# Kernel tuning notes

Hardware: AMD Instinct MI355X
Metric: run time of the kernel (lower is better)

## Reference

```python
import jax, jax.numpy as jnp
import numpy as np


def setup_inputs() -> dict:
    key = jax.random.key(0)
    k1, k2, k3 = jax.random.split(key, 3)
    N, F, C, E = 100000, 256, 64, 3200000
    x = jax.random.normal(k1, (N, F), dtype=jnp.float32)
    edge_index = jax.random.randint(k2, (2, E), 0, N, dtype=jnp.int64)
    W = jax.random.normal(k3, (F, C), dtype=jnp.float32) * (1.0 / np.sqrt(F))
    b = jnp.zeros((C,), dtype=jnp.float32)
    return {"x": x, "edge_index": edge_index, "W": W, "b": b}


def reference(x, edge_index, W, b):
    N = x.shape[0]
    # Linear transform first (GCNConv: x @ W)
    xw = x @ W  # [N, C]
    # gcn_norm: add self-loops with weight 1
    loops = jnp.arange(N, dtype=edge_index.dtype)
    src = jnp.concatenate([edge_index[0], loops])
    dst = jnp.concatenate([edge_index[1], loops])
    ones = jnp.ones(src.shape[0], dtype=xw.dtype)
    deg = jax.ops.segment_sum(ones, dst, num_segments=N)  # in-degree incl. self-loop
    deg_inv_sqrt = jnp.where(deg > 0, jax.lax.rsqrt(deg), 0.0)
    norm = deg_inv_sqrt[src] * deg_inv_sqrt[dst]  # [E+N]
    # Message: norm * x_j, then MEAN aggregation over destinations (aggr='mean')
    msg = xw[src] * norm[:, None]  # [E+N, C]
    agg = jax.ops.segment_sum(msg, dst, num_segments=N)  # [N, C]
    cnt = jnp.maximum(deg, 1.0)  # number of incoming messages per node
    out = agg / cnt[:, None] + b
    return jax.nn.log_softmax(out, axis=1)
```

## Files before the change

kernel.cpp:

```cpp
#include <hip/hip_runtime.h>


#define C_DIM 64
#define F_DIM 256
#define TILE 128
#define BIN_PT 16
#define BIN_TILE_E 4096
#define SORT_CAP 6144
#define SMEM_BYTES 36880

typedef __attribute__((ext_vector_type(8))) short bf16x8;
typedef __attribute__((ext_vector_type(2))) short bf16x2;
typedef __attribute__((ext_vector_type(4))) float f32x4;

static __device__ __forceinline__ unsigned short f2bf(float f) {
    unsigned int u = __float_as_uint(f);
    unsigned int r = (u + 0x7FFFu + ((u >> 16) & 1u)) >> 16;
    return (unsigned short)r;
}
static __device__ __forceinline__ float u2lo(unsigned int u) {
    return __uint_as_float(u << 16);
}
static __device__ __forceinline__ float u2hi(unsigned int u) {
    return __uint_as_float(u & 0xFFFF0000u);
}

#if __has_builtin(__builtin_amdgcn_fdot2_f32_bf16)
static __device__ __forceinline__ void acc_pair(unsigned int u, float& lo, float& hi) {
    union { unsigned int ui; bf16x2 v; } p;
    p.ui = u;
    const bf16x2 SEL_LO = { (short)0x3F80, (short)0 };
    const bf16x2 SEL_HI = { (short)0, (short)0x3F80 };
    lo = __builtin_amdgcn_fdot2_f32_bf16(p.v, SEL_LO, lo, false);
    hi = __builtin_amdgcn_fdot2_f32_bf16(p.v, SEL_HI, hi, false);
}
#else
static __device__ __forceinline__ void acc_pair(unsigned int u, float& lo, float& hi) {
    lo += u2lo(u);
    hi += u2hi(u);
}
#endif


__global__ void k_zero1(int* __restrict__ a, int N) {
    int i = blockIdx.x * blockDim.x + threadIdx.x;
    if (i < N) a[i] = 0;
}

__global__ void k_zero2(int* __restrict__ a, int* __restrict__ b, int N) {
    int i = blockIdx.x * blockDim.x + threadIdx.x;
    if (i < N) { a[i] = 0; b[i] = 0; }
}

__global__ void k_count(const int* __restrict__ ei, int* __restrict__ degE, int E) {
    int stride = gridDim.x * blockDim.x;
    for (int e = blockIdx.x * blockDim.x + threadIdx.x; e < E; e += stride)
        atomicAdd(&degE[ei[E + e]], 1);
}

__global__ void k_dis2(const int* __restrict__ degE, float* __restrict__ dis, int N) {
    int i = blockIdx.x * blockDim.x + threadIdx.x;
    if (i < N) dis[i] = rsqrtf((float)(degE[i] + 1));
}


__global__ void k_prep(const float* __restrict__ W, unsigned short* __restrict__ Wt,
                       int* __restrict__ gcur, int K) {
    int i = blockIdx.x * blockDim.x + threadIdx.x;
    int c = i & 63, k = i >> 6;
    Wt[(size_t)c * F_DIM + k] = f2bf(W[(size_t)k * C_DIM + c]);
    if (i < K) gcur[i] = i * SORT_CAP;
}


__launch_bounds__(256)
__global__ void k_bin_gemm(const int* __restrict__ ei, int* __restrict__ gcur,
                           unsigned int* __restrict__ colb,
                           const float* __restrict__ x,
                           const unsigned short* __restrict__ Wt,
                           unsigned short* __restrict__ yb,
                           int E, int K, int nTiles, int N) {
    __shared__ __align__(16) char smem[SMEM_BYTES];
    const int t = threadIdx.x;

    if (blockIdx.x < nTiles) {
        int* hcnt  = (int*)smem;
        int* hoff  = (int*)(smem + 4096);
        int* gbase = (int*)(smem + 8192);
        int* wps   = (int*)(smem + 12288);
        unsigned int*  stage    = (unsigned int*)(smem + 12304);
        unsigned short* stage_bk = (unsigned short*)(smem + 28688);
        const int wv = t >> 6;
        const int ln = t & 63;

        const int e0 = blockIdx.x * BIN_TILE_E;
        const int nE = min(BIN_TILE_E, E - e0);
        hcnt[t] = 0; hcnt[t + 256] = 0; hcnt[t + 512] = 0; hcnt[t + 768] = 0;
        __syncthreads();

        unsigned int pk[BIN_PT];
        int bk[BIN_PT];
        int off[BIN_PT];
        #pragma unroll
        for (int j = 0; j < BIN_PT; ++j) {
            int e = e0 + j * 256 + t;
            if (e < E) {
                int s = ei[e];
                int d = ei[E + e];
                int k = d >> 7;
                bk[j]  = k;
                pk[j]  = ((unsigned)(d & 127) << 25) | (unsigned)s;
                off[j] = atomicAdd(&hcnt[k], 1);
            } else bk[j] = -1;
        }
        __syncthreads();

        int a0 = hcnt[t*4], a1 = hcnt[t*4+1], a2 = hcnt[t*4+2], a3 = hcnt[t*4+3];
        int s4 = a0 + a1 + a2 + a3;
        int incl = s4;
        #pragma unroll
        for (int o = 1; o < 64; o <<= 1) {
            int u = __shfl_up(incl, o, 64);
            if (ln >= o) incl += u;
        }
        if (ln == 63) wps[wv] = incl;
        __syncthreads();
        int wpre = 0;
        #pragma unroll
        for (int w = 0; w < 4; ++w)
            if (w < wv) wpre += wps[w];
        int eb = wpre + incl - s4;
        hoff[t*4+0] = eb;
        hoff[t*4+1] = eb + a0;
        hoff[t*4+2] = eb + a0 + a1;
        hoff[t*4+3] = eb + a0 + a1 + a2;
        __syncthreads();

        #pragma unroll
        for (int j = 0; j < BIN_PT; ++j)
            if (bk[j] >= 0) {
                int p = hoff[bk[j]] + off[j];
                stage[p] = pk[j];
                stage_bk[p] = (unsigned short)bk[j];
            }

        for (int kq = t; kq < K; kq += 256) {
            int c = hcnt[kq];
            gbase[kq] = (c > 0) ? atomicAdd(&gcur[kq], c) : 0;
        }
        __syncthreads();

        for (int i = t; i < nE; i += 256) {
            int bb = stage_bk[i];
            int idx = gbase[bb] + (i - hoff[bb]);
            if (idx < (bb + 1) * SORT_CAP)
                colb[idx] = stage[i];
        }
        return;
    }

    float4 (*xs2)[1024] = (float4 (*)[1024])smem;
    const int wv   = t >> 6;
    const int lane = t & 63;
    const int lr   = lane & 15;
    const int lq   = lane >> 4;
    const int row0 = (blockIdx.x - nTiles) * 64;

    auto stagefn = [&](int buf, int kk) {
        #pragma unroll
        for (int j = 0; j < 4; ++j) {
            int base_idx = j * 256 + wv * 64;
            int idx = base_idx + lane;
            int r   = idx >> 4;
            int c4  = idx & 15;
            int sc4 = c4 ^ (r & 15);
            int gr  = row0 + r;
            if (gr >= N) gr = N - 1;
            const float* g = x + (size_t)gr * F_DIM + kk * 64 + sc4 * 4;
            float4* lbase = &xs2[buf][base_idx];
            __builtin_amdgcn_global_load_lds(
                (const __attribute__((address_space(1))) unsigned int*)g,
                (__attribute__((address_space(3))) unsigned int*)lbase,
                16, 0, 0);
        }
    };

    f32x4 acc[4] = {};

    stagefn(0, 0);
    __syncthreads();

    for (int kk = 0; kk < 4; ++kk) {
        if (kk < 3) stagefn((kk + 1) & 1, kk + 1);

        const float4* rowp = &xs2[kk & 1][(wv * 16 + lr) * 16];
        #pragma unroll
        for (int kc2 = 0; kc2 < 2; ++kc2) {
            int c4 = kc2 * 8 + lq * 2;
            float4 f0 = rowp[c4 ^ lr];
            float4 f1 = rowp[(c4 + 1) ^ lr];
            union { bf16x8 v; unsigned int u[4]; } a;
            a.u[0] = (unsigned)f2bf(f0.x) | ((unsigned)f2bf(f0.y) << 16);
            a.u[1] = (unsigned)f2bf(f0.z) | ((unsigned)f2bf(f0.w) << 16);
            a.u[2] = (unsigned)f2bf(f1.x) | ((unsigned)f2bf(f1.y) << 16);
            a.u[3] = (unsigned)f2bf(f1.z) | ((unsigned)f2bf(f1.w) << 16);
            const int kglob = kk * 64 + kc2 * 32 + lq * 8;
            #pragma unroll
            for (int cb = 0; cb < 4; ++cb) {
                bf16x8 bfr = *(const bf16x8*)(Wt + (size_t)(cb * 16 + lr) * F_DIM + kglob);
                acc[cb] = __builtin_amdgcn_mfma_f32_16x16x32_bf16(a.v, bfr, acc[cb], 0, 0, 0);
            }
        }
        __syncthreads();
    }

    const int rbase = row0 + wv * 16 + lq * 4;
    #pragma unroll
    for (int j = 0; j < 4; ++j) {
        int r = rbase + j;
        if (r < N) {
            #pragma unroll
            for (int cb = 0; cb < 4; ++cb)
                yb[(size_t)r * C_DIM + cb * 16 + lr] = f2bf(acc[cb][j]);
        }
    }
}


__launch_bounds__(256)
__global__ void k_sort(unsigned int* __restrict__ colb,
                       const int* __restrict__ gcur,
                       int* __restrict__ rowptr, int* __restrict__ rowcnt,
                       float* __restrict__ dis,
                       unsigned int* __restrict__ yb2,
                       int N, int K) {
    __shared__ unsigned int scache[SORT_CAP];
    __shared__ int ncnt[TILE];
    __shared__ int nscan[TILE];
    __shared__ int ncur[TILE];
    __shared__ float sdis[TILE];
    const int t = threadIdx.x;
    const int k = blockIdx.x;
    const int base = k * SORT_CAP;
    const int cnt  = min(gcur[k] - base, SORT_CAP);
    const int node0 = k << 7;

    if (t < TILE) ncnt[t] = 0;
    __syncthreads();
    for (int i = t; i < cnt; i += 256) {
        unsigned int pk = colb[base + i];
        scache[i] = pk;
        atomicAdd(&ncnt[pk >> 25], 1);
    }
    __syncthreads();

    if (t < TILE) nscan[t] = ncnt[t];
    __syncthreads();
    for (int o = 1; o < TILE; o <<= 1) {
        int v = 0;
        if (t < TILE && t >= o) v = nscan[t - o];
        __syncthreads();
        if (t < TILE) nscan[t] += v;
        __syncthreads();
    }
    if (t < TILE) {
        int ex = nscan[t] - ncnt[t];
        ncur[t] = ex;
        int node = node0 + t;
        if (node < N) {
            rowptr[node] = base + ex;
            rowcnt[node] = ncnt[t];
            float d = rsqrtf((float)(ncnt[t] + 1));
            dis[node] = d;
            sdis[t] = d;
        }
    }
    __syncthreads();

    for (int i = t; i < cnt; i += 256) {
        unsigned int pk = scache[i];
        int dl  = (int)(pk >> 25);
        int pos = atomicAdd(&ncur[dl], 1);
        colb[base + pos] = pk & 0x1FFFFFFu;
    }

    const int nrows = min(TILE, N - node0);
    unsigned int* yrow = yb2 + (size_t)node0 * 32;
    for (int u = t; u < nrows * 32; u += 256) {
        int r = u >> 5;
        unsigned int v = yrow[u];
        float d = sdis[r];
        unsigned short lo = f2bf(u2lo(v) * d);
        unsigned short hi = f2bf(u2hi(v) * d);
        yrow[u] = ((unsigned int)hi << 16) | lo;
    }
}


__launch_bounds__(256)
__global__ void k_agg(const int* __restrict__ rowptr, const int* __restrict__ rowcnt,
                      const int* __restrict__ col,
                      const uint4* __restrict__ yb8, const float* __restrict__ dis,
                      const float* __restrict__ b, float* __restrict__ out, int N) {
    const int lane = threadIdx.x & 63;
    const int g    = lane >> 3;
    const int cl   = lane & 7;
    int row = blockIdx.x * 4 + (threadIdx.x >> 6);
    if (row >= N) return;
    const int start = rowptr[row];
    const int cntE  = rowcnt[row];
    const int end   = start + cntE;

    float a0 = 0.f, a1 = 0.f, a2 = 0.f, a3 = 0.f;
    float a4 = 0.f, a5 = 0.f, a6 = 0.f, a7 = 0.f;
    if (g == 0) {
        uint4 u = yb8[(size_t)row * 8 + cl];
        a0 = u2lo(u.x); a1 = u2hi(u.x); a2 = u2lo(u.y); a3 = u2hi(u.y);
        a4 = u2lo(u.z); a5 = u2hi(u.z); a6 = u2lo(u.w); a7 = u2hi(u.w);
    }

    int i = start + g;
    for (; i + 24 < end; i += 32) {
        int s[4];
        #pragma unroll
        for (int j = 0; j < 4; ++j) s[j] = col[i + 8 * j];
        uint4 v[4];
        #pragma unroll
        for (int j = 0; j < 4; ++j) v[j] = yb8[(size_t)s[j] * 8 + cl];
        #pragma unroll
        for (int j = 0; j < 4; ++j) {
            acc_pair(v[j].x, a0, a1);
            acc_pair(v[j].y, a2, a3);
            acc_pair(v[j].z, a4, a5);
            acc_pair(v[j].w, a6, a7);
        }
    }
    for (; i + 8 < end; i += 16) {
        int s0 = col[i], s1 = col[i + 8];
        uint4 v0 = yb8[(size_t)s0 * 8 + cl];
        uint4 v1 = yb8[(size_t)s1 * 8 + cl];
        acc_pair(v0.x, a0, a1); acc_pair(v1.x, a0, a1);
        acc_pair(v0.y, a2, a3); acc_pair(v1.y, a2, a3);
        acc_pair(v0.z, a4, a5); acc_pair(v1.z, a4, a5);
        acc_pair(v0.w, a6, a7); acc_pair(v1.w, a6, a7);
    }
    for (; i < end; i += 8) {
        uint4 u = yb8[(size_t)col[i] * 8 + cl];
        acc_pair(u.x, a0, a1);
        acc_pair(u.y, a2, a3);
        acc_pair(u.z, a4, a5);
        acc_pair(u.w, a6, a7);
    }

    #pragma unroll
    for (int o = 8; o <= 32; o <<= 1) {
        a0 += __shfl_xor(a0, o, 64); a1 += __shfl_xor(a1, o, 64);
        a2 += __shfl_xor(a2, o, 64); a3 += __shfl_xor(a3, o, 64);
        a4 += __shfl_xor(a4, o, 64); a5 += __shfl_xor(a5, o, 64);
        a6 += __shfl_xor(a6, o, 64); a7 += __shfl_xor(a7, o, 64);
    }

    const float scale = dis[row] / (float)(cntE + 1);
    const float4 b0 = *(const float4*)&b[8 * cl];
    const float4 b1 = *(const float4*)&b[8 * cl + 4];
    float v0 = a0 * scale + b0.x;
    float v1 = a1 * scale + b0.y;
    float v2 = a2 * scale + b0.z;
    float v3 = a3 * scale + b0.w;
    float v4 = a4 * scale + b1.x;
    float v5 = a5 * scale + b1.y;
    float v6 = a6 * scale + b1.z;
    float v7 = a7 * scale + b1.w;

    float m = fmaxf(fmaxf(fmaxf(v0, v1), fmaxf(v2, v3)),
                    fmaxf(fmaxf(v4, v5), fmaxf(v6, v7)));
    #pragma unroll
    for (int o = 4; o >= 1; o >>= 1) m = fmaxf(m, __shfl_xor(m, o, 64));
    float ss = __expf(v0 - m) + __expf(v1 - m) + __expf(v2 - m) + __expf(v3 - m)
             + __expf(v4 - m) + __expf(v5 - m) + __expf(v6 - m) + __expf(v7 - m);
    #pragma unroll
    for (int o = 4; o >= 1; o >>= 1) ss += __shfl_xor(ss, o, 64);
    float lg = logf(ss);

    if (g == 0) {
        float* orow = out + (size_t)row * C_DIM + 8 * cl;
        *(float4*)(orow + 0) = make_float4(v0 - m - lg, v1 - m - lg, v2 - m - lg, v3 - m - lg);
        *(float4*)(orow + 4) = make_float4(v4 - m - lg, v5 - m - lg, v6 - m - lg, v7 - m - lg);
    }
}


__launch_bounds__(256, 4)
__global__ void k_gemmF(const float* __restrict__ x, const float* __restrict__ W,
                        const float* __restrict__ dis, float* __restrict__ y, int N) {
    __shared__ float xs[64 * 68];
    __shared__ float ws[64 * 64];
    const int t   = threadIdx.x;
    const int c16 = t & 15;
    const int rg  = t >> 4;
    const int row0 = blockIdx.x * 64;

    float acc[4][4] = {};

    for (int kk = 0; kk < F_DIM / 64; ++kk) {
        {
            int r  = t >> 2;
            int fq = (t & 3) * 16;
            int grow = row0 + r;
            float4 v0, v1, v2, v3;
            if (grow < N) {
                const float* src = x + (long long)grow * F_DIM + kk * 64 + fq;
                v0 = *(const float4*)(src + 0);
                v1 = *(const float4*)(src + 4);
                v2 = *(const float4*)(src + 8);
                v3 = *(const float4*)(src + 12);
            } else {
                v0 = v1 = v2 = v3 = make_float4(0.f, 0.f, 0.f, 0.f);
            }
            float4* dstp = (float4*)&xs[r * 68 + fq];
            dstp[0] = v0; dstp[1] = v1; dstp[2] = v2; dstp[3] = v3;
        }
        {
            int f  = t >> 2;
            int cq = (t & 3) * 16;
            const float* src = W + (long long)(kk * 64 + f) * C_DIM + cq;
            float4* dstp = (float4*)&ws[f * 64 + cq];
            dstp[0] = *(const float4*)(src + 0);
            dstp[1] = *(const float4*)(src + 4);
            dstp[2] = *(const float4*)(src + 8);
            dstp[3] = *(const float4*)(src + 12);
        }
        __syncthreads();

        const float4* xs4 = (const float4*)xs;
        const float4* ws4 = (const float4*)ws;
        #pragma unroll
        for (int f4 = 0; f4 < 16; ++f4) {
            float xr[4][4];
            #pragma unroll
            for (int k = 0; k < 4; ++k) {
                float4 v = xs4[(rg * 4 + k) * 17 + f4];
                xr[k][0] = v.x; xr[k][1] = v.y; xr[k][2] = v.z; xr[k][3] = v.w;
            }
            #pragma unroll
            for (int j = 0; j < 4; ++j) {
                float4 wv = ws4[(f4 * 4 + j) * 16 + c16];
                #pragma unroll
                for (int k = 0; k < 4; ++k) {
                    acc[k][0] += xr[k][j] * wv.x;
                    acc[k][1] += xr[k][j] * wv.y;
                    acc[k][2] += xr[k][j] * wv.z;
                    acc[k][3] += xr[k][j] * wv.w;
                }
            }
        }
        __syncthreads();
    }

    const int c = c16 * 4;
    #pragma unroll
    for (int k = 0; k < 4; ++k) {
        int row = row0 + rg * 4 + k;
        if (row < N) {
            float dd = dis[row];
            float4 v = make_float4(acc[k][0]*dd, acc[k][1]*dd, acc[k][2]*dd, acc[k][3]*dd);
            *(float4*)&y[(size_t)row * C_DIM + c] = v;
        }
    }
}

__global__ void k_scan_blk(const int* __restrict__ degE, int* __restrict__ excl,
                           int* __restrict__ bsum, int N) {
    __shared__ int sm[1024];
    const int tid = threadIdx.x;
    int i = blockIdx.x * 1024 + tid;
    int v = (i < N) ? degE[i] : 0;
    sm[tid] = v;
    __syncthreads();
    for (int off = 1; off < 1024; off <<= 1) {
        int t = (tid >= off) ? sm[tid - off] : 0;
        __syncthreads();
        sm[tid] += t;
        __syncthreads();
    }
    int incl = sm[tid];
    if (i < N) excl[i] = incl - v;
    if (tid == 1023) bsum[blockIdx.x] = incl;
}

__global__ void k_scan_top(int* __restrict__ bs, int nblk) {
    __shared__ int sm[128];
    const int tid = threadIdx.x;
    int v = (tid < nblk) ? bs[tid] : 0;
    sm[tid] = v;
    __syncthreads();
    for (int off = 1; off < 128; off <<= 1) {
        int t = (tid >= off) ? sm[tid - off] : 0;
        __syncthreads();
        sm[tid] += t;
        __syncthreads();
    }
    if (tid < nblk) bs[tid] = sm[tid] - v;
}

__global__ void k_scan_add(const int* __restrict__ excl, const int* __restrict__ bs,
                           int* __restrict__ rowptr, int N, int E) {
    int i = blockIdx.x * blockDim.x + threadIdx.x;
    if (i < N) rowptr[i] = excl[i] + bs[i >> 10];
    if (i == 0) rowptr[N] = E;
}

__global__ void k_scatter(const int* __restrict__ ei, const int* __restrict__ rowptr,
                          int* __restrict__ cnt, int* __restrict__ col, int E) {
    int stride = gridDim.x * blockDim.x;
    for (int e = blockIdx.x * blockDim.x + threadIdx.x; e < E; e += stride) {
        int s = ei[e];
        int d = ei[E + e];
        int p = atomicAdd(&cnt[d], 1);
        col[rowptr[d] + p] = s;
    }
}

__global__ void k_aggB(const int* __restrict__ rowptr, const int* __restrict__ col,
                       const float* __restrict__ y, const float* __restrict__ dis,
                       const float* __restrict__ b, float* __restrict__ out, int N) {
    const int lane = threadIdx.x & 63;
    int row = blockIdx.x * 4 + (threadIdx.x >> 6);
    if (row >= N) return;
    const int start = rowptr[row], end = rowptr[row + 1];
    float acc = y[(size_t)row * C_DIM + lane];
    for (int i = start; i < end; ++i) acc += y[(size_t)col[i] * C_DIM + lane];
    float val = acc * dis[row] / (float)(end - start + 1) + b[lane];
    float m = val;
    #pragma unroll
    for (int o = 32; o >= 1; o >>= 1) m = fmaxf(m, __shfl_xor(m, o, 64));
    float ex = expf(val - m);
    float ss = ex;
    #pragma unroll
    for (int o = 32; o >= 1; o >>= 1) ss += __shfl_xor(ss, o, 64);
    out[(size_t)row * C_DIM + lane] = val - m - logf(ss);
}

__global__ void k_selfloop2(const float* __restrict__ y, const float* __restrict__ dis,
                            float* __restrict__ agg, int NC) {
    int i = blockIdx.x * blockDim.x + threadIdx.x;
    if (i < NC) agg[i] = dis[i >> 6] * y[i];
}

__launch_bounds__(256)
__global__ void k_edge2(const int* __restrict__ ei, const float* __restrict__ y,
                        const float* __restrict__ dis, float* __restrict__ agg, int E) {
    const int lane = threadIdx.x & 63;
    int wid = (blockIdx.x * blockDim.x + threadIdx.x) >> 6;
    int nw  = (gridDim.x * blockDim.x) >> 6;
    for (int e = wid; e < E; e += nw) {
        int s = ei[e];
        int d = ei[E + e];
        atomicAdd(&agg[(size_t)d * C_DIM + lane], y[(size_t)s * C_DIM + lane] * dis[d]);
    }
}

__launch_bounds__(256)
__global__ void k_final2(float* __restrict__ agg, const int* __restrict__ degE,
                         const float* __restrict__ b, int N) {
    const int lane = threadIdx.x & 63;
    int row = blockIdx.x * 4 + (threadIdx.x >> 6);
    if (row >= N) return;
    float v = agg[(size_t)row * C_DIM + lane] / (float)(degE[row] + 1) + b[lane];
    float m = v;
    #pragma unroll
    for (int o = 32; o >= 1; o >>= 1) m = fmaxf(m, __shfl_xor(m, o, 64));
    float ex = expf(v - m);
    float ss = ex;
    #pragma unroll
    for (int o = 32; o >= 1; o >>= 1) ss += __shfl_xor(ss, o, 64);
    agg[(size_t)row * C_DIM + lane] = v - m - logf(ss);
}


extern "C" void kernel_launch(void* const* d_in, const int* in_sizes, int n_in,
                              void* d_out, int out_size, void* d_ws, size_t ws_size,
                              hipStream_t stream) {
    const float* x  = (const float*)d_in[0];
    const int*   ei = (const int*)d_in[1];
    const float* W  = (const float*)d_in[2];
    const float* b  = (const float*)d_in[3];

    const int C = in_sizes[3];
    const int F = in_sizes[2] / C;
    const int N = in_sizes[0] / F;
    const int E = in_sizes[1] / 2;

    float* out = (float*)d_out;
    char*  wsb = (char*)d_ws;

    const int K    = (N + TILE - 1) / TILE;
    const int nblk = (N + 1023) / 1024;

    size_t offA = 0;
    unsigned short* yb = (unsigned short*)(wsb + offA); offA += ((size_t)N * C * 2 + 15) & ~15ull;
    unsigned short* Wt = (unsigned short*)(wsb + offA); offA += ((size_t)F * C * 2 + 15) & ~15ull;
    float* disA   = (float*)(wsb + offA); offA += (size_t)N * 4;
    int*   rowptrA= (int*)(wsb + offA);   offA += (size_t)N * 4;
    int*   rowcntA= (int*)(wsb + offA);   offA += (size_t)N * 4;
    int*   gcur   = (int*)(wsb + offA);   offA += (size_t)K * 4;
    unsigned int* colb = (unsigned int*)(wsb + offA); offA += (size_t)K * SORT_CAP * 4;

    size_t offB = 0;
    float* yB     = (float*)(wsb + offB); offB += (size_t)N * C * 4;
    float* disB   = (float*)(wsb + offB); offB += (size_t)N * 4;
    int*   rowptrB= (int*)(wsb + offB);   offB += ((size_t)N + 1) * 4;
    int*   degE   = (int*)(wsb + offB);   offB += (size_t)N * 4;
    int*   cntB   = (int*)(wsb + offB);   offB += (size_t)N * 4;
    int*   excl   = (int*)(wsb + offB);   offB += (size_t)nblk * 1024 * 4;
    int*   bsum   = (int*)(wsb + offB);   offB += 128 * 4;
    int*   colB   = (int*)(wsb + offB);   offB += (size_t)E * 4;

    const bool okA = (offA <= ws_size) && (K <= 1024) && (N < (1 << 25)) &&
                     (C == 64) && (F == 256) &&
                     ((long long)E < (long long)K * SORT_CAP);
    const bool okB = (offB <= ws_size) && (nblk <= 128);

    const dim3 B256(256);
    const dim3 gN((N + 255) / 256);
    const int nTiles = (E + BIN_TILE_E - 1) / BIN_TILE_E;
    const int gemmBlocks = (N + 63) / 64;

    if (okA) {
        hipLaunchKernelGGL(k_prep,     dim3((F * C + 255) / 256), B256, 0, stream,
                           W, Wt, gcur, K);
        hipLaunchKernelGGL(k_bin_gemm, dim3(nTiles + gemmBlocks), B256, 0, stream,
                           ei, gcur, colb, x, Wt, yb, E, K, nTiles, N);
        hipLaunchKernelGGL(k_sort,     dim3(K), B256, 0, stream, colb, gcur,
                           rowptrA, rowcntA, disA, (unsigned int*)yb, N, K);
        hipLaunchKernelGGL(k_agg,      dim3((N + 3) / 4), B256, 0, stream,
                           rowptrA, rowcntA, (const int*)colb,
                           (const uint4*)yb, disA, b, out, N);
    } else if (okB) {
        hipLaunchKernelGGL(k_zero2,    gN, B256, 0, stream, degE, cntB, N);
        hipLaunchKernelGGL(k_count,    dim3(2048), B256, 0, stream, ei, degE, E);
        hipLaunchKernelGGL(k_dis2,     gN, B256, 0, stream, degE, disB, N);
        hipLaunchKernelGGL(k_scan_blk, dim3(nblk), dim3(1024), 0, stream, degE, excl, bsum, N);
        hipLaunchKernelGGL(k_scan_top, dim3(1), dim3(128), 0, stream, bsum, nblk);
        hipLaunchKernelGGL(k_scan_add, gN, B256, 0, stream, excl, bsum, rowptrB, N, E);
        hipLaunchKernelGGL(k_gemmF,    dim3(gemmBlocks), B256, 0, stream, x, W, disB, yB, N);
        hipLaunchKernelGGL(k_scatter,  dim3(2048), B256, 0, stream, ei, rowptrB, cntB, colB, E);
        hipLaunchKernelGGL(k_aggB,     dim3((N + 3) / 4), B256, 0, stream,
                           rowptrB, colB, yB, disB, b, out, N);
    } else {
        hipLaunchKernelGGL(k_zero1,     gN, B256, 0, stream, degE, N);
        hipLaunchKernelGGL(k_count,     dim3(2048), B256, 0, stream, ei, degE, E);
        hipLaunchKernelGGL(k_dis2,      gN, B256, 0, stream, degE, disB, N);
        hipLaunchKernelGGL(k_gemmF,     dim3(gemmBlocks), B256, 0, stream, x, W, disB, yB, N);
        hipLaunchKernelGGL(k_selfloop2, dim3(((size_t)N * C + 255) / 256), B256, 0, stream,
                           yB, disB, out, N * C);
        hipLaunchKernelGGL(k_edge2,     dim3(4096), B256, 0, stream, ei, yB, disB, out, E);
        hipLaunchKernelGGL(k_final2,    dim3((N + 3) / 4), B256, 0, stream, out, degE, b, N);
    }
}
```

Before: 160.0 us.

## Store transformed features as FP8 to halve gather traffic in aggregation

When the FP8 conversion builtins are available, the GEMM output xw is written as FP8 instead of bf16, the degree scaling in k_sort rescales FP8 values in place, and the aggregation kernel gathers 8-byte FP8 rows and accumulates with packed f32x2 conversions. This halves the bytes per gathered neighbour row in the random-access aggregation. The GEMM blocks are also moved ahead of the binning blocks in the fused launch so they are scheduled first. FP8 precision (e4m3, from two rounding steps) risks exceeding accuracy tolerances on the log-softmax output.

Result: faster. 148.3 us (-7.3%).

```diff
diff --git a/kernel.cpp b/kernel.cpp
--- a/kernel.cpp
+++ b/kernel.cpp
@@ -9,9 +9,14 @@
 #define SORT_CAP 6144
 #define SMEM_BYTES 36880
 
+#if __has_builtin(__builtin_amdgcn_cvt_pk_f32_fp8) && __has_builtin(__builtin_amdgcn_cvt_pk_fp8_f32)
+#define USE_FP8 1
+#endif
+
 typedef __attribute__((ext_vector_type(8))) short bf16x8;
 typedef __attribute__((ext_vector_type(2))) short bf16x2;
 typedef __attribute__((ext_vector_type(4))) float f32x4;
+typedef __attribute__((ext_vector_type(2))) float f32x2;
 
 static __device__ __forceinline__ unsigned short f2bf(float f) {
     unsigned int u = __float_as_uint(f);
@@ -25,6 +30,7 @@
     return __uint_as_float(u & 0xFFFF0000u);
 }
 
+#if !defined(USE_FP8)
 #if __has_builtin(__builtin_amdgcn_fdot2_f32_bf16)
 static __device__ __forceinline__ void acc_pair(unsigned int u, float& lo, float& hi) {
     union { unsigned int ui; bf16x2 v; } p;
@@ -40,6 +46,7 @@
     hi += u2hi(u);
 }
 #endif
+#endif
 
 
 __global__ void k_zero1(int* __restrict__ a, int N) {
@@ -78,12 +85,92 @@
                            unsigned int* __restrict__ colb,
                            const float* __restrict__ x,
                            const unsigned short* __restrict__ Wt,
-                           unsigned short* __restrict__ yb,
-                           int E, int K, int nTiles, int N) {
+                           void* __restrict__ yout,
+                           int E, int K, int nTiles, int gemmBlocks, int N) {
     __shared__ __align__(16) char smem[SMEM_BYTES];
     const int t = threadIdx.x;
 
-    if (blockIdx.x < nTiles) {
+    if (blockIdx.x < gemmBlocks) {
+        float4 (*xs2)[1024] = (float4 (*)[1024])smem;
+        const int wv   = t >> 6;
+        const int lane = t & 63;
+        const int lr   = lane & 15;
+        const int lq   = lane >> 4;
+        const int row0 = blockIdx.x * 64;
+
+        auto stagefn = [&](int buf, int kk) {
+            #pragma unroll
+            for (int j = 0; j < 4; ++j) {
+                int base_idx = j * 256 + wv * 64;
+                int idx = base_idx + lane;
+                int r   = idx >> 4;
+                int c4  = idx & 15;
+                int sc4 = c4 ^ (r & 15);
+                int gr  = row0 + r;
+                if (gr >= N) gr = N - 1;
+                const float* g = x + (size_t)gr * F_DIM + kk * 64 + sc4 * 4;
+                float4* lbase = &xs2[buf][base_idx];
+                __builtin_amdgcn_global_load_lds(
+                    (const __attribute__((address_space(1))) unsigned int*)g,
+                    (__attribute__((address_space(3))) unsigned int*)lbase,
+                    16, 0, 0);
+            }
+        };
+
+        f32x4 acc[4] = {};
+
+        stagefn(0, 0);
+        __syncthreads();
+
+        for (int kk = 0; kk < 4; ++kk) {
+            if (kk < 3) stagefn((kk + 1) & 1, kk + 1);
+
+            const float4* rowp = &xs2[kk & 1][(wv * 16 + lr) * 16];
+            #pragma unroll
+            for (int kc2 = 0; kc2 < 2; ++kc2) {
+                int c4 = kc2 * 8 + lq * 2;
+                float4 f0 = rowp[c4 ^ lr];
+                float4 f1 = rowp[(c4 + 1) ^ lr];
+                union { bf16x8 v; unsigned int u[4]; } a;
+                a.u[0] = (unsigned)f2bf(f0.x) | ((unsigned)f2bf(f0.y) << 16);
+                a.u[1] = (unsigned)f2bf(f0.z) | ((unsigned)f2bf(f0.w) << 16);
+                a.u[2] = (unsigned)f2bf(f1.x) | ((unsigned)f2bf(f1.y) << 16);
+                a.u[3] = (unsigned)f2bf(f1.z) | ((unsigned)f2bf(f1.w) << 16);
+                const int kglob = kk * 64 + kc2 * 32 + lq * 8;
+                #pragma unroll
+                for (int cb = 0; cb < 4; ++cb) {
+                    bf16x8 bfr = *(const bf16x8*)(Wt + (size_t)(cb * 16 + lr) * F_DIM + kglob);
+                    acc[cb] = __builtin_amdgcn_mfma_f32_16x16x32_bf16(a.v, bfr, acc[cb], 0, 0, 0);
+                }
+            }
+            __syncthreads();
+        }
+
+        const int rbase = row0 + wv * 16 + lq * 4;
+        #pragma unroll
+        for (int j = 0; j < 4; ++j) {
+            int r = rbase + j;
+            if (r < N) {
+#ifdef USE_FP8
+                unsigned char* yf = (unsigned char*)yout;
+                #pragma unroll
+                for (int cb = 0; cb < 4; ++cb) {
+                    float v = acc[cb][j];
+                    int p = __builtin_amdgcn_cvt_pk_fp8_f32(v, v, 0, false);
+                    yf[(size_t)r * C_DIM + cb * 16 + lr] = (unsigned char)(p & 0xFF);
+                }
+#else
+                unsigned short* ybp = (unsigned short*)yout;
+                #pragma unroll
+                for (int cb = 0; cb < 4; ++cb)
+                    ybp[(size_t)r * C_DIM + cb * 16 + lr] = f2bf(acc[cb][j]);
+#endif
+            }
+        }
+        return;
+    }
+
+    {
         int* hcnt  = (int*)smem;
         int* hoff  = (int*)(smem + 4096);
         int* gbase = (int*)(smem + 8192);
@@ -93,7 +180,7 @@
         const int wv = t >> 6;
         const int ln = t & 63;
 
-        const int e0 = blockIdx.x * BIN_TILE_E;
+        const int e0 = (blockIdx.x - gemmBlocks) * BIN_TILE_E;
         const int nE = min(BIN_TILE_E, E - e0);
         hcnt[t] = 0; hcnt[t + 256] = 0; hcnt[t + 512] = 0; hcnt[t + 768] = 0;
         __syncthreads();
@@ -156,73 +243,6 @@
             if (idx < (bb + 1) * SORT_CAP)
                 colb[idx] = stage[i];
         }
-        return;
-    }
-
-    float4 (*xs2)[1024] = (float4 (*)[1024])smem;
-    const int wv   = t >> 6;
-    const int lane = t & 63;
-    const int lr   = lane & 15;
-    const int lq   = lane >> 4;
-    const int row0 = (blockIdx.x - nTiles) * 64;
-
-    auto stagefn = [&](int buf, int kk) {
-        #pragma unroll
-        for (int j = 0; j < 4; ++j) {
-            int base_idx = j * 256 + wv * 64;
-            int idx = base_idx + lane;
-            int r   = idx >> 4;
-            int c4  = idx & 15;
-            int sc4 = c4 ^ (r & 15);
-            int gr  = row0 + r;
-            if (gr >= N) gr = N - 1;
-            const float* g = x + (size_t)gr * F_DIM + kk * 64 + sc4 * 4;
-            float4* lbase = &xs2[buf][base_idx];
-            __builtin_amdgcn_global_load_lds(
-                (const __attribute__((address_space(1))) unsigned int*)g,
-                (__attribute__((address_space(3))) unsigned int*)lbase,
-                16, 0, 0);
-        }
-    };
-
-    f32x4 acc[4] = {};
-
-    stagefn(0, 0);
-    __syncthreads();
-
-    for (int kk = 0; kk < 4; ++kk) {
-        if (kk < 3) stagefn((kk + 1) & 1, kk + 1);
-
-        const float4* rowp = &xs2[kk & 1][(wv * 16 + lr) * 16];
-        #pragma unroll
-        for (int kc2 = 0; kc2 < 2; ++kc2) {
-            int c4 = kc2 * 8 + lq * 2;
-            float4 f0 = rowp[c4 ^ lr];
-            float4 f1 = rowp[(c4 + 1) ^ lr];
-            union { bf16x8 v; unsigned int u[4]; } a;
-            a.u[0] = (unsigned)f2bf(f0.x) | ((unsigned)f2bf(f0.y) << 16);
-            a.u[1] = (unsigned)f2bf(f0.z) | ((unsigned)f2bf(f0.w) << 16);
-            a.u[2] = (unsigned)f2bf(f1.x) | ((unsigned)f2bf(f1.y) << 16);
-            a.u[3] = (unsigned)f2bf(f1.z) | ((unsigned)f2bf(f1.w) << 16);
-            const int kglob = kk * 64 + kc2 * 32 + lq * 8;
-            #pragma unroll
-            for (int cb = 0; cb < 4; ++cb) {
-                bf16x8 bfr = *(const bf16x8*)(Wt + (size_t)(cb * 16 + lr) * F_DIM + kglob);
-                acc[cb] = __builtin_amdgcn_mfma_f32_16x16x32_bf16(a.v, bfr, acc[cb], 0, 0, 0);
-            }
-        }
-        __syncthreads();
-    }
-
-    const int rbase = row0 + wv * 16 + lq * 4;
-    #pragma unroll
-    for (int j = 0; j < 4; ++j) {
-        int r = rbase + j;
-        if (r < N) {
-            #pragma unroll
-            for (int cb = 0; cb < 4; ++cb)
-                yb[(size_t)r * C_DIM + cb * 16 + lr] = f2bf(acc[cb][j]);
-        }
     }
 }
 
@@ -232,7 +252,7 @@
                        const int* __restrict__ gcur,
                        int* __restrict__ rowptr, int* __restrict__ rowcnt,
                        float* __restrict__ dis,
-                       unsigned int* __restrict__ yb2,
+                       unsigned int* __restrict__ yw,
                        int N, int K) {
     __shared__ unsigned int scache[SORT_CAP];
     __shared__ int ncnt[TILE];
@@ -285,7 +305,20 @@
     }
 
     const int nrows = min(TILE, N - node0);
-    unsigned int* yrow = yb2 + (size_t)node0 * 32;
+#ifdef USE_FP8
+    unsigned int* yrow = yw + (size_t)node0 * 16;
+    for (int u = t; u < nrows * 16; u += 256) {
+        int r = u >> 4;
+        float d = sdis[r];
+        unsigned int v = yrow[u];
+        f32x2 lo = __builtin_amdgcn_cvt_pk_f32_fp8((int)v, false);
+        f32x2 hi = __builtin_amdgcn_cvt_pk_f32_fp8((int)v, true);
+        int p = __builtin_amdgcn_cvt_pk_fp8_f32(lo.x * d, lo.y * d, 0, false);
+        p = __builtin_amdgcn_cvt_pk_fp8_f32(hi.x * d, hi.y * d, p, true);
+        yrow[u] = (unsigned int)p;
+    }
+#else
+    unsigned int* yrow = yw + (size_t)node0 * 32;
     for (int u = t; u < nrows * 32; u += 256) {
         int r = u >> 5;
         unsigned int v = yrow[u];
@@ -294,13 +327,14 @@
         unsigned short hi = f2bf(u2hi(v) * d);
         yrow[u] = ((unsigned int)hi << 16) | lo;
     }
+#endif
 }
 
 
 __launch_bounds__(256)
 __global__ void k_agg(const int* __restrict__ rowptr, const int* __restrict__ rowcnt,
                       const int* __restrict__ col,
-                      const uint4* __restrict__ yb8, const float* __restrict__ dis,
+                      const void* __restrict__ yin, const float* __restrict__ dis,
                       const float* __restrict__ b, float* __restrict__ out, int N) {
     const int lane = threadIdx.x & 63;
     const int g    = lane >> 3;
@@ -311,22 +345,59 @@
     const int cntE  = rowcnt[row];
     const int end   = start + cntE;
 
-    float a0 = 0.f, a1 = 0.f, a2 = 0.f, a3 = 0.f;
-    float a4 = 0.f, a5 = 0.f, a6 = 0.f, a7 = 0.f;
+    float a0, a1, a2, a3, a4, a5, a6, a7;
+
+#ifdef USE_FP8
+    const uint2* yv = (const uint2*)yin;
+    f32x2 p01 = {0.f, 0.f}, p23 = {0.f, 0.f}, p45 = {0.f, 0.f}, p67 = {0.f, 0.f};
     if (g == 0) {
-        uint4 u = yb8[(size_t)row * 8 + cl];
-        a0 = u2lo(u.x); a1 = u2hi(u.x); a2 = u2lo(u.y); a3 = u2hi(u.y);
-        a4 = u2lo(u.z); a5 = u2hi(u.z); a6 = u2lo(u.w); a7 = u2hi(u.w);
-    }
-
+        uint2 u = yv[(size_t)row * 8 + cl];
+        p01 = __builtin_amdgcn_cvt_pk_f32_fp8((int)u.x, false);
+        p23 = __builtin_amdgcn_cvt_pk_f32_fp8((int)u.x, true);
+        p45 = __builtin_amdgcn_cvt_pk_f32_fp8((int)u.y, false);
+        p67 = __builtin_amdgcn_cvt_pk_f32_fp8((int)u.y, true);
+    }
     int i = start + g;
     for (; i + 24 < end; i += 32) {
         int s[4];
         #pragma unroll
         for (int j = 0; j < 4; ++j) s[j] = col[i + 8 * j];
+        uint2 v[4];
+        #pragma unroll
+        for (int j = 0; j < 4; ++j) v[j] = yv[(size_t)s[j] * 8 + cl];
+        #pragma unroll
+        for (int j = 0; j < 4; ++j) {
+            p01 += __builtin_amdgcn_cvt_pk_f32_fp8((int)v[j].x, false);
+            p23 += __builtin_amdgcn_cvt_pk_f32_fp8((int)v[j].x, true);
+            p45 += __builtin_amdgcn_cvt_pk_f32_fp8((int)v[j].y, false);
+            p67 += __builtin_amdgcn_cvt_pk_f32_fp8((int)v[j].y, true);
+        }
+    }
+    for (; i < end; i += 8) {
+        uint2 u = yv[(size_t)col[i] * 8 + cl];
+        p01 += __builtin_amdgcn_cvt_pk_f32_fp8((int)u.x, false);
+        p23 += __builtin_amdgcn_cvt_pk_f32_fp8((int)u.x, true);
+        p45 += __builtin_amdgcn_cvt_pk_f32_fp8((int)u.y, false);
+        p67 += __builtin_amdgcn_cvt_pk_f32_fp8((int)u.y, true);
+    }
+    a0 = p01.x; a1 = p01.y; a2 = p23.x; a3 = p23.y;
+    a4 = p45.x; a5 = p45.y; a6 = p67.x; a7 = p67.y;
+#else
+    const uint4* yv = (const uint4*)yin;
+    a0 = a1 = a2 = a3 = a4 = a5 = a6 = a7 = 0.f;
+    if (g == 0) {
+        uint4 u = yv[(size_t)row * 8 + cl];
+        a0 = u2lo(u.x); a1 = u2hi(u.x); a2 = u2lo(u.y); a3 = u2hi(u.y);
+        a4 = u2lo(u.z); a5 = u2hi(u.z); a6 = u2lo(u.w); a7 = u2hi(u.w);
+    }
+    int i = start + g;
+    for (; i + 24 < end; i += 32) {
+        int s[4];
+        #pragma unroll
+        for (int j = 0; j < 4; ++j) s[j] = col[i + 8 * j];
         uint4 v[4];
         #pragma unroll
-        for (int j = 0; j < 4; ++j) v[j] = yb8[(size_t)s[j] * 8 + cl];
+        for (int j = 0; j < 4; ++j) v[j] = yv[(size_t)s[j] * 8 + cl];
         #pragma unroll
         for (int j = 0; j < 4; ++j) {
             acc_pair(v[j].x, a0, a1);
@@ -335,22 +406,14 @@
             acc_pair(v[j].w, a6, a7);
         }
     }
-    for (; i + 8 < end; i += 16) {
-        int s0 = col[i], s1 = col[i + 8];
-        uint4 v0 = yb8[(size_t)s0 * 8 + cl];
-        uint4 v1 = yb8[(size_t)s1 * 8 + cl];
-        acc_pair(v0.x, a0, a1); acc_pair(v1.x, a0, a1);
-        acc_pair(v0.y, a2, a3); acc_pair(v1.y, a2, a3);
-        acc_pair(v0.z, a4, a5); acc_pair(v1.z, a4, a5);
-        acc_pair(v0.w, a6, a7); acc_pair(v1.w, a6, a7);
-    }
     for (; i < end; i += 8) {
-        uint4 u = yb8[(size_t)col[i] * 8 + cl];
+        uint4 u = yv[(size_t)col[i] * 8 + cl];
         acc_pair(u.x, a0, a1);
         acc_pair(u.y, a2, a3);
         acc_pair(u.z, a4, a5);
         acc_pair(u.w, a6, a7);
     }
+#endif
 
     #pragma unroll
     for (int o = 8; o <= 32; o <<= 1) {
@@ -598,7 +661,7 @@
     const int nblk = (N + 1023) / 1024;
 
     size_t offA = 0;
-    unsigned short* yb = (unsigned short*)(wsb + offA); offA += ((size_t)N * C * 2 + 15) & ~15ull;
+    void*  yv   = (void*)(wsb + offA);    offA += ((size_t)N * C * 2 + 15) & ~15ull;
     unsigned short* Wt = (unsigned short*)(wsb + offA); offA += ((size_t)F * C * 2 + 15) & ~15ull;
     float* disA   = (float*)(wsb + offA); offA += (size_t)N * 4;
     int*   rowptrA= (int*)(wsb + offA);   offA += (size_t)N * 4;
@@ -629,13 +692,13 @@
     if (okA) {
         hipLaunchKernelGGL(k_prep,     dim3((F * C + 255) / 256), B256, 0, stream,
                            W, Wt, gcur, K);
-        hipLaunchKernelGGL(k_bin_gemm, dim3(nTiles + gemmBlocks), B256, 0, stream,
-                           ei, gcur, colb, x, Wt, yb, E, K, nTiles, N);
+        hipLaunchKernelGGL(k_bin_gemm, dim3(gemmBlocks + nTiles), B256, 0, stream,
+                           ei, gcur, colb, x, Wt, yv, E, K, nTiles, gemmBlocks, N);
         hipLaunchKernelGGL(k_sort,     dim3(K), B256, 0, stream, colb, gcur,
-                           rowptrA, rowcntA, disA, (unsigned int*)yb, N, K);
+                           rowptrA, rowcntA, disA, (unsigned int*)yv, N, K);
         hipLaunchKernelGGL(k_agg,      dim3((N + 3) / 4), B256, 0, stream,
                            rowptrA, rowcntA, (const int*)colb,
-                           (const uint4*)yb, disA, b, out, N);
+                           (const void*)yv, disA, b, out, N);
     } else if (okB) {
         hipLaunchKernelGGL(k_zero2,    gN, B256, 0, stream, degE, cntB, N);
         hipLaunchKernelGGL(k_count,    dim3(2048), B256, 0, stream, ei, degE, E);
```
